# Kernel optimization log

Measured on AMD Instinct MI355X. Metric: run time of the kernel, lower is better.

The kernel has to match this reference:

```python
import jax, jax.numpy as jnp
import numpy as np

E, S, L, H, C = 32, 64, 20, 512, 32  # episodes, steps, max_comm_len, hidden_size, comm_shape
STD_MIN, STD_MAX = 2.0611536e-09, 7.389056  # exp(-20), exp(2)


def setup_inputs() -> dict:
    key = jax.random.key(0)
    ks = jax.random.split(key, 12)
    def p(k, shape):
        return jax.random.normal(k, shape, jnp.float32) * 0.02
    return {
        'x': jax.random.normal(ks[0], (E, S, H), jnp.float32),
        'Wr': p(ks[1], (2 * H, H)), 'br': jnp.zeros((H,), jnp.float32),
        'Wz': p(ks[2], (2 * H, H)), 'bz': jnp.zeros((H,), jnp.float32),
        'Wn': p(ks[3], (2 * H, H)), 'bn': jnp.zeros((H,), jnp.float32),
        'conv_w1': p(ks[4], (H // 4, H, 1)), 'conv_b1': jnp.zeros((H // 4,), jnp.float32),
        'conv_w3': p(ks[5], (H // 4, H, 3)), 'conv_b3': jnp.zeros((H // 4,), jnp.float32),
        'conv_w5': p(ks[6], (H // 4, H, 5)), 'conv_b5': jnp.zeros((H // 4,), jnp.float32),
        'conv_w7': p(ks[7], (H // 4, H, 7)), 'conv_b7': jnp.zeros((H // 4,), jnp.float32),
        'prelu_a': jnp.asarray(0.25, jnp.float32),
        'W_mu': p(ks[8], (H, C)), 'b_mu': jnp.zeros((C,), jnp.float32),
        'W_std': p(ks[9], (H, C)), 'b_std': jnp.zeros((C,), jnp.float32),
        'eps': jax.random.normal(ks[10], (E, S, L, C), jnp.float32),
    }


def reference(x, Wr, br, Wz, bz, Wn, bn,
              conv_w1, conv_b1, conv_w3, conv_b3, conv_w5, conv_b5, conv_w7, conv_b7,
              prelu_a, W_mu, b_mu, W_std, b_std, eps):
    B = E * S
    xf = x.reshape(B, H)  # same input fed to the RNN at every comm step

    def step(h, _):
        xh = jnp.concatenate([xf, h], -1)
        r = jax.nn.sigmoid(xh @ Wr + br)
        z = jax.nn.sigmoid(xh @ Wz + bz)
        n = jnp.tanh(jnp.concatenate([xf, r * h], -1) @ Wn + bn)
        h_new = (1.0 - z) * n + z * h  # time_constant=1 -> h = new GRU state
        return h_new, h_new

    h0 = jnp.zeros((B, H), x.dtype)
    _, hs = jax.lax.scan(step, h0, None, length=L)  # (L, B, H)
    comm_h = jnp.transpose(hs, (1, 2, 0))  # (B, H, L) -- NCW layout for conv

    dn = ('NCH', 'OIH', 'NCH')
    def conv(w, b, k):
        pad = (k - 1) // 2
        y = jax.lax.conv_general_dilated(comm_h, w, (1,), [(pad, pad)], dimension_numbers=dn)
        return y + b[None, :, None]

    y = jnp.concatenate([
        conv(conv_w1, conv_b1, 1),
        conv(conv_w3, conv_b3, 3),
        conv(conv_w5, conv_b5, 5),
        conv(conv_w7, conv_b7, 7),
    ], axis=1)  # (B, H, L)
    y = jnp.where(y >= 0, y, prelu_a * y)  # PReLU; dropout is identity in eval
    y = jnp.transpose(y, (0, 2, 1)).reshape(E, S, L, H)

    mu = y @ W_mu + b_mu
    std = jnp.clip(jax.nn.softplus(y @ W_std + b_std), STD_MIN, STD_MAX)
    comm = mu + eps * std  # reparameterized Normal sample
    comm_out = jnp.tanh(comm)
    log2pi = jnp.asarray(np.log(2.0 * np.pi), jnp.float32)
    log_prob = (-0.5 * ((comm - mu) / std) ** 2 - jnp.log(std) - 0.5 * log2pi
                - jnp.log(1.0 - comm_out ** 2 + 1e-6))
    log_prob = jnp.mean(log_prob, -1, keepdims=True)  # (E,S,L,1)
    log_prob = jnp.mean(log_prob, -2)  # (E,S,1)
    return comm_out, log_prob
```

## Files before the change

kernel.cpp:

```cpp
#include <hip/hip_runtime.h>
#include <hip/hip_bf16.h>

typedef __hip_bfloat16 bf16;
typedef short short8 __attribute__((ext_vector_type(8)));
typedef float floatx4 __attribute__((ext_vector_type(4)));

#define BDIM 2048
#define HDIM 512
#define LDIM 20
#define CDIM 32
#define LSTR 40

__device__ __forceinline__ float sigm(float x) { return 1.0f / (1.0f + expf(-x)); }

__device__ __forceinline__ void ll16(const short* g, short* l)
{
    __builtin_amdgcn_global_load_lds(
        (const __attribute__((address_space(1))) void*)g,
        (__attribute__((address_space(3))) void*)l, 16, 0, 0);
}
#define WAITVM(N) asm volatile("s_waitcnt vmcnt(" #N ")" ::: "memory")

__device__ __forceinline__ void gemm_tile_k(
    const short* __restrict__ A, int lda,
    const short* __restrict__ Bt, int ldb,
    int K, short* lds, floatx4 (&acc)[4][4], int tid)
{
    short* As = lds;
    short* Bs = lds + 128 * LSTR;
    const int wave = tid >> 6, lane = tid & 63;
    const int wm = wave & 1, wn = wave >> 1;
    const int m16 = lane & 15, quad = lane >> 4;
    const int r0 = tid >> 2;
    const int koff = (tid & 3) * 8;

    short8 a0 = *(const short8*)(A + (size_t)r0 * lda + koff);
    short8 a1 = *(const short8*)(A + (size_t)(r0 + 64) * lda + koff);
    short8 b0 = *(const short8*)(Bt + (size_t)r0 * ldb + koff);
    short8 b1 = *(const short8*)(Bt + (size_t)(r0 + 64) * ldb + koff);
    for (int k0 = 0; k0 < K; k0 += 32) {
        __syncthreads();
        *(short8*)(As + r0 * LSTR + koff) = a0;
        *(short8*)(As + (r0 + 64) * LSTR + koff) = a1;
        *(short8*)(Bs + r0 * LSTR + koff) = b0;
        *(short8*)(Bs + (r0 + 64) * LSTR + koff) = b1;
        __syncthreads();
        if (k0 + 32 < K) {
            a0 = *(const short8*)(A + (size_t)r0 * lda + k0 + 32 + koff);
            a1 = *(const short8*)(A + (size_t)(r0 + 64) * lda + k0 + 32 + koff);
            b0 = *(const short8*)(Bt + (size_t)r0 * ldb + k0 + 32 + koff);
            b1 = *(const short8*)(Bt + (size_t)(r0 + 64) * ldb + k0 + 32 + koff);
        }
        short8 af[4], bfr[4];
#pragma unroll
        for (int i = 0; i < 4; ++i)
            af[i] = *(short8*)(As + (wm * 64 + i * 16 + m16) * LSTR + quad * 8);
#pragma unroll
        for (int j = 0; j < 4; ++j)
            bfr[j] = *(short8*)(Bs + (wn * 64 + j * 16 + m16) * LSTR + quad * 8);
#pragma unroll
        for (int i = 0; i < 4; ++i)
#pragma unroll
            for (int j = 0; j < 4; ++j)
                acc[i][j] = __builtin_amdgcn_mfma_f32_16x16x32_bf16(
                    af[i], bfr[j], acc[i][j], 0, 0, 0);
    }
}

__device__ __forceinline__ void gemm_tile_k256(
    const short* __restrict__ A,
    const short* __restrict__ Bt,
    short* lds, floatx4 (&acc)[4][4], int tid)
{
    short* As = lds;
    short* Bs = lds + 256 * LSTR;
    const int wave = tid >> 6, lane = tid & 63;
    const int wm = wave & 3, wn = wave >> 2;
    const int m16 = lane & 15, quad = lane >> 4;
    const int r0 = tid >> 2;
    const int koff = (tid & 3) * 8;

    short8 a0 = *(const short8*)(A + (size_t)r0 * 512 + koff);
    short8 a1 = *(const short8*)(A + (size_t)(r0 + 128) * 512 + koff);
    short8 b0 = *(const short8*)(Bt + (size_t)r0 * 512 + koff);
    for (int k0 = 0; k0 < 512; k0 += 32) {
        __syncthreads();
        *(short8*)(As + r0 * LSTR + koff) = a0;
        *(short8*)(As + (r0 + 128) * LSTR + koff) = a1;
        *(short8*)(Bs + r0 * LSTR + koff) = b0;
        __syncthreads();
        if (k0 + 32 < 512) {
            a0 = *(const short8*)(A + (size_t)r0 * 512 + k0 + 32 + koff);
            a1 = *(const short8*)(A + (size_t)(r0 + 128) * 512 + k0 + 32 + koff);
            b0 = *(const short8*)(Bt + (size_t)r0 * 512 + k0 + 32 + koff);
        }
        short8 af[4], bfr[4];
#pragma unroll
        for (int i = 0; i < 4; ++i)
            af[i] = *(short8*)(As + (wm * 64 + i * 16 + m16) * LSTR + quad * 8);
#pragma unroll
        for (int j = 0; j < 4; ++j)
            bfr[j] = *(short8*)(Bs + (wn * 64 + j * 16 + m16) * LSTR + quad * 8);
#pragma unroll
        for (int i = 0; i < 4; ++i)
#pragma unroll
            for (int j = 0; j < 4; ++j)
                acc[i][j] = __builtin_amdgcn_mfma_f32_16x16x32_bf16(
                    af[i], bfr[j], acc[i][j], 0, 0, 0);
    }
}

__global__ __launch_bounds__(256) void k_prep_xb(const float* __restrict__ x,
                                                 bf16* __restrict__ xb)
{
    int i = blockIdx.x * 256 + threadIdx.x;
    xb[i] = (bf16)x[i];
}

__global__ __launch_bounds__(256) void k_transpose_512(const float* __restrict__ src,
                                                       bf16* __restrict__ dst)
{
    __shared__ float tile[32][33];
    int tx = threadIdx.x & 31, ty = threadIdx.x >> 5;
    int k0 = blockIdx.x * 32, n0 = blockIdx.y * 32;
#pragma unroll
    for (int i = 0; i < 32; i += 8)
        tile[ty + i][tx] = src[(size_t)(k0 + ty + i) * 512 + n0 + tx];
    __syncthreads();
#pragma unroll
    for (int i = 0; i < 32; i += 8)
        dst[(size_t)(n0 + ty + i) * 512 + k0 + tx] = (bf16)tile[tx][ty + i];
}

__global__ __launch_bounds__(256) void k_swzW(const float* __restrict__ Wr,
                                              const float* __restrict__ Wz,
                                              const float* __restrict__ Wn,
                                              bf16* __restrict__ Wfrag)
{
    int idx = blockIdx.x * 256 + threadIdx.x;
    int e = idx & 7, lane = (idx >> 3) & 63;
    int t2 = idx >> 9;
    int f = t2 % 6, jk = t2 / 6;
    int kc = jk & 15, j = jk >> 4;
    int ftype = f >> 1;
    int col = j * 32 + (f & 1) * 16 + (lane & 15);
    int k = kc * 32 + ((lane >> 4) << 3) + e;
    const float* W = (ftype == 0) ? Wr : (ftype == 1) ? Wz : Wn;
    Wfrag[idx] = (bf16)W[(size_t)(512 + k) * 512 + col];
}

__global__ __launch_bounds__(256) void k_prep_wc(
    const float* __restrict__ w1, const float* __restrict__ w3,
    const float* __restrict__ w5, const float* __restrict__ w7,
    bf16* __restrict__ wt)
{
    int idx = blockIdx.x * 256 + threadIdx.x;
    int g, base;
    if (idx < 65536)       { g = 0; base = 0;      }
    else if (idx < 262144) { g = 1; base = 65536;  }
    else if (idx < 589824) { g = 2; base = 262144; }
    else                   { g = 3; base = 589824; }
    int rel = idx - base;
    int k = 2 * g + 1;
    int ci = rel & 511;
    int t2 = rel >> 9;
    int co = t2 & 127;
    int tap = t2 >> 7;
    const float* w = (g == 0) ? w1 : (g == 1) ? w3 : (g == 2) ? w5 : w7;
    wt[idx] = (bf16)w[((size_t)co * 512 + ci) * k + tap];
}

__global__ __launch_bounds__(256) void k_prep_wh(const float* __restrict__ Wmu,
                                                 const float* __restrict__ Wstd,
                                                 bf16* __restrict__ Wh_t)
{
    int idx = blockIdx.x * 256 + threadIdx.x;
    int n = idx >> 9, k = idx & 511;
    float v = (n < 32) ? Wmu[(size_t)k * 32 + n] : Wstd[(size_t)k * 32 + (n - 32)];
    Wh_t[idx] = (bf16)v;
}

__global__ __launch_bounds__(256) void k_gx(
    const bf16* __restrict__ xb, const bf16* __restrict__ Wx_t,
    const float* __restrict__ br, const float* __restrict__ bz,
    const float* __restrict__ bn, bf16* __restrict__ gxb)
{
    __shared__ short lds[2 * 128 * LSTR];
    const int tid = threadIdx.x;
    const int row0 = blockIdx.x * 128, col0 = blockIdx.y * 128;
    floatx4 acc[4][4];
#pragma unroll
    for (int i = 0; i < 4; ++i)
#pragma unroll
        for (int j = 0; j < 4; ++j) acc[i][j] = (floatx4)0.0f;
    gemm_tile_k((const short*)xb + (size_t)row0 * 512, 512,
                (const short*)Wx_t + (size_t)col0 * 512, 512, 512, lds, acc, tid);
    const int wave = tid >> 6, lane = tid & 63;
    const int wm = wave & 1, wn = wave >> 1;
    const int m16 = lane & 15, quad = lane >> 4;
#pragma unroll
    for (int i = 0; i < 4; ++i)
#pragma unroll
        for (int j = 0; j < 4; ++j)
#pragma unroll
            for (int reg = 0; reg < 4; ++reg) {
                int b = row0 + wm * 64 + i * 16 + quad * 4 + reg;
                int n = col0 + wn * 64 + j * 16 + m16;
                float bias = (n < 512) ? br[n] : (n < 1024) ? bz[n - 512] : bn[n - 1024];
                gxb[(size_t)b * 1536 + n] = (bf16)(acc[i][j][reg] + bias);
            }
}

__device__ __forceinline__ void gbar2(unsigned* flags, int j, unsigned target,
                                      bool fast, int tid)
{
    WAITVM(0);
    __syncthreads();
    if (tid < 64) {
        if (tid == 0) {
            if (!fast) __threadfence();
            __hip_atomic_store(flags + j, target, __ATOMIC_RELAXED,
                               __HIP_MEMORY_SCOPE_AGENT);
        }
        unsigned v; int guard = 0;
        do {
            v = (tid < 16) ? __hip_atomic_load(flags + tid, __ATOMIC_RELAXED,
                                               __HIP_MEMORY_SCOPE_AGENT)
                           : target;
        } while (__ballot(v >= target) != ~0ull && ++guard < (1 << 20));
        if (!fast) { if (tid == 0) __threadfence(); }
        else asm volatile("buffer_inv" ::: "memory");
    }
    __syncthreads();
}

template<int NF>
__device__ __forceinline__ void phase_reg(
    const short* __restrict__ srcw, const short* __restrict__ wl,
    int f0, int lane, floatx4 (&acc)[NF])
{
    const short* g = srcw + (size_t)(lane & 15) * 512 + (lane >> 4) * 8;
    short8 a[16];
#pragma unroll
    for (int kc = 0; kc < 16; ++kc)
        a[kc] = *(const short8*)(g + kc * 32);
#pragma unroll
    for (int kc = 0; kc < 16; ++kc) {
        short8 bfr[NF];
#pragma unroll
        for (int f = 0; f < NF; ++f)
            bfr[f] = *(short8*)(wl + ((kc * 6 + f0 + f) << 9) + lane * 8);
#pragma unroll
        for (int f = 0; f < NF; ++f)
            acc[f] = __builtin_amdgcn_mfma_f32_16x16x32_bf16(a[kc], bfr[f],
                                                             acc[f], 0, 0, 0);
    }
}

__global__ __launch_bounds__(512, 2) void k_gru9(
    const bf16* __restrict__ Wfrag, const bf16* __restrict__ gxb,
    bf16* __restrict__ hs, bf16* __restrict__ rhb,
    unsigned* __restrict__ ctr, int* __restrict__ xcdtab)
{
    __shared__ short wlds[6 * 16 * 512];
    const int tid = threadIdx.x;
    const int wave = tid >> 6, lane = tid & 63;
    const int m16 = lane & 15, quad = lane >> 4;
    const int b = blockIdx.x;
    const int s = b >> 3;
    const int m = (b & 7) + ((s & 1) << 3);
    const int j = s >> 1;
    const int wrow = wave * 16;
    unsigned* flg  = ctr + m * 32;
    unsigned* vflg = ctr + m * 32 + 16;

    int myxcd;
    asm volatile("s_getreg_b32 %0, hwreg(HW_REG_XCC_ID)" : "=s"(myxcd));
    myxcd &= 15;
    if (tid == 0) xcdtab[m * 16 + j] = myxcd;

    const short* wsrc = (const short*)Wfrag + (size_t)j * 49152;
#pragma unroll
    for (int r = 0; r < 12; ++r)
        ll16(wsrc + ((wave * 12 + r) << 9) + lane * 8, wlds + ((wave * 12 + r) << 9));

    float gxr[2][4], gxz[2][4], gxn[2][4];
#pragma unroll
    for (int reg = 0; reg < 4; ++reg) {
        const bf16* gp = gxb + (size_t)(m * 128 + wrow + quad * 4 + reg) * 1536 + j * 32;
#pragma unroll
        for (int fc = 0; fc < 2; ++fc) {
            int c = fc * 16 + m16;
            gxr[fc][reg] = __bfloat162float(gp[c]);
            gxz[fc][reg] = __bfloat162float(gp[512 + c]);
            gxn[fc][reg] = __bfloat162float(gp[1024 + c]);
        }
    }

    gbar2(vflg, j, 1u, false, tid);
    bool fast = true;
#pragma unroll
    for (int jj = 0; jj < 16; ++jj) {
        int xv = __hip_atomic_load((const int*)xcdtab + m * 16 + jj,
                                   __ATOMIC_RELAXED, __HIP_MEMORY_SCOPE_AGENT);
        fast = fast && (xv == myxcd);
    }

    float h32[2][4];
    float zf[2][4];
    unsigned nbar = 0;
    const int rowg = m * 128 + wrow + quad * 4;

#pragma unroll
    for (int fc = 0; fc < 2; ++fc)
#pragma unroll
        for (int reg = 0; reg < 4; ++reg) {
            float z = sigm(gxz[fc][reg]);
            float nv = tanhf(gxn[fc][reg]);
            float hn = (1.0f - z) * nv;
            h32[fc][reg] = hn;
            hs[(size_t)(rowg + reg) * 512 + j * 32 + fc * 16 + m16] = (bf16)hn;
        }
    ++nbar; gbar2(flg, j, nbar, fast, tid);

    for (int t = 1; t < LDIM; ++t) {
        floatx4 acc[4];
#pragma unroll
        for (int f = 0; f < 4; ++f) acc[f] = (floatx4)0.0f;
        phase_reg<4>((const short*)hs + ((size_t)(t - 1) * BDIM + m * 128 + wrow) * 512,
                     wlds, 0, lane, acc);
#pragma unroll
        for (int fc = 0; fc < 2; ++fc)
#pragma unroll
            for (int reg = 0; reg < 4; ++reg) {
                float r = sigm(acc[fc][reg] + gxr[fc][reg]);
                zf[fc][reg] = sigm(acc[2 + fc][reg] + gxz[fc][reg]);
                rhb[(size_t)(rowg + reg) * 512 + j * 32 + fc * 16 + m16] =
                    (bf16)(r * h32[fc][reg]);
            }
        ++nbar; gbar2(flg, j, nbar, fast, tid);
        floatx4 acc2[2];
#pragma unroll
        for (int f = 0; f < 2; ++f) acc2[f] = (floatx4)0.0f;
        phase_reg<2>((const short*)rhb + (size_t)(m * 128 + wrow) * 512,
                     wlds, 4, lane, acc2);
#pragma unroll
        for (int fc = 0; fc < 2; ++fc)
#pragma unroll
            for (int reg = 0; reg < 4; ++reg) {
                float nv = tanhf(acc2[fc][reg] + gxn[fc][reg]);
                float z = zf[fc][reg];
                float hn = (1.0f - z) * nv + z * h32[fc][reg];
                h32[fc][reg] = hn;
                hs[((size_t)t * BDIM + rowg + reg) * 512 + j * 32 + fc * 16 + m16] =
                    (bf16)hn;
            }
        if (t < LDIM - 1) { ++nbar; gbar2(flg, j, nbar, fast, tid); }
    }
}

__global__ __launch_bounds__(512, 2) void k_conv(
    const bf16* __restrict__ hs, const bf16* __restrict__ Wc_t,
    const float* __restrict__ b1, const float* __restrict__ b3,
    const float* __restrict__ b5, const float* __restrict__ b7,
    const float* __restrict__ pa, bf16* __restrict__ y)
{
    __shared__ short lds[(256 + 128) * LSTR];
    const int tid = threadIdx.x;
    const int btile = blockIdx.x, g = blockIdx.y, l = blockIdx.z;
    const int row0 = btile * 256;
    const int ktap = 2 * g + 1, p = g;
    const int offs[4] = {0, 65536, 262144, 589824};
    const short* Wg = (const short*)Wc_t + offs[g];
    floatx4 acc[4][4];
#pragma unroll
    for (int i = 0; i < 4; ++i)
#pragma unroll
        for (int j = 0; j < 4; ++j) acc[i][j] = (floatx4)0.0f;
    for (int tap = 0; tap < ktap; ++tap) {
        int li = l + tap - p;
        if (li < 0 || li >= LDIM) continue;
        gemm_tile_k256((const short*)hs + (size_t)li * BDIM * HDIM + (size_t)row0 * 512,
                       Wg + (size_t)tap * 128 * 512, lds, acc, tid);
    }
    const float* bp = (g == 0) ? b1 : (g == 1) ? b3 : (g == 2) ? b5 : b7;
    const float a = *pa;
    const int wave = tid >> 6, lane = tid & 63;
    const int wm = wave & 3, wn = wave >> 2;
    const int m16 = lane & 15, quad = lane >> 4;
#pragma unroll
    for (int i = 0; i < 4; ++i)
#pragma unroll
        for (int j = 0; j < 4; ++j)
#pragma unroll
            for (int reg = 0; reg < 4; ++reg) {
                int b = row0 + wm * 64 + i * 16 + quad * 4 + reg;
                int col = wn * 64 + j * 16 + m16;
                float v = acc[i][j][reg] + bp[col];
                v = (v >= 0.0f) ? v : a * v;
                y[((size_t)b * LDIM + l) * 512 + g * 128 + col] = (bf16)v;
            }
}

__global__ __launch_bounds__(256) void k_head2(
    const bf16* __restrict__ y, const bf16* __restrict__ Wh_t,
    const float* __restrict__ bmu, const float* __restrict__ bstd,
    const float* __restrict__ eps, float* __restrict__ out_comm,
    float* __restrict__ lpsum)
{
    __shared__ short As[128 * LSTR];
    __shared__ short Bs[64 * LSTR];
    const int tid = threadIdx.x;
    const int wave = tid >> 6, lane = tid & 63;
    const int m16 = lane & 15, quad = lane >> 4;
    const int r0 = tid >> 2, koff = (tid & 3) * 8;
    const int row0 = blockIdx.x * 128;
    floatx4 acc[2][4];
#pragma unroll
    for (int i = 0; i < 2; ++i)
#pragma unroll
        for (int j = 0; j < 4; ++j) acc[i][j] = (floatx4)0.0f;
    const short* Ap = (const short*)y + (size_t)row0 * 512;
    const short* Bp = (const short*)Wh_t;
    short8 ga0 = *(const short8*)(Ap + (size_t)r0 * 512 + koff);
    short8 ga1 = *(const short8*)(Ap + (size_t)(r0 + 64) * 512 + koff);
    short8 gb0 = *(const short8*)(Bp + (size_t)r0 * 512 + koff);
    for (int k0 = 0; k0 < 512; k0 += 32) {
        __syncthreads();
        *(short8*)(As + r0 * LSTR + koff) = ga0;
        *(short8*)(As + (r0 + 64) * LSTR + koff) = ga1;
        *(short8*)(Bs + r0 * LSTR + koff) = gb0;
        __syncthreads();
        if (k0 + 32 < 512) {
            ga0 = *(const short8*)(Ap + (size_t)r0 * 512 + k0 + 32 + koff);
            ga1 = *(const short8*)(Ap + (size_t)(r0 + 64) * 512 + k0 + 32 + koff);
            gb0 = *(const short8*)(Bp + (size_t)r0 * 512 + k0 + 32 + koff);
        }
        short8 af[2], bfr[4];
#pragma unroll
        for (int i = 0; i < 2; ++i)
            af[i] = *(short8*)(As + (wave * 32 + i * 16 + m16) * LSTR + quad * 8);
#pragma unroll
        for (int j = 0; j < 4; ++j)
            bfr[j] = *(short8*)(Bs + (j * 16 + m16) * LSTR + quad * 8);
#pragma unroll
        for (int i = 0; i < 2; ++i)
#pragma unroll
            for (int j = 0; j < 4; ++j)
                acc[i][j] = __builtin_amdgcn_mfma_f32_16x16x32_bf16(
                    af[i], bfr[j], acc[i][j], 0, 0, 0);
    }
#pragma unroll
    for (int i = 0; i < 2; ++i)
#pragma unroll
        for (int reg = 0; reg < 4; ++reg) {
            int row = row0 + wave * 32 + i * 16 + quad * 4 + reg;
            float lp = 0.0f;
#pragma unroll
            for (int jj = 0; jj < 2; ++jj) {
                int c = jj * 16 + m16;
                float mu = acc[i][jj][reg] + bmu[c];
                float sraw = acc[i][jj + 2][reg] + bstd[c];
                float sp = (sraw > 20.0f) ? sraw : log1pf(expf(sraw));
                float sd = fminf(fmaxf(sp, 2.0611536e-09f), 7.389056f);
                float e = eps[(size_t)row * 32 + c];
                float comm = fmaf(e, sd, mu);
                float tt = tanhf(comm);
                out_comm[(size_t)row * 32 + c] = tt;
                lp += -0.5f * e * e - logf(sd) - 0.91893853320467274f
                      - logf(1.0f - tt * tt + 1e-6f);
            }
            lp += __shfl_xor(lp, 1, 16);
            lp += __shfl_xor(lp, 2, 16);
            lp += __shfl_xor(lp, 4, 16);
            lp += __shfl_xor(lp, 8, 16);
            if (m16 == 0) lpsum[row] = lp;
        }
}

__global__ __launch_bounds__(256) void k_final(const float* __restrict__ lpsum,
                                               float* __restrict__ out2)
{
    int b = blockIdx.x * 256 + threadIdx.x;
    if (b < BDIM) {
        float s = 0.0f;
#pragma unroll
        for (int i = 0; i < LDIM; ++i) s += lpsum[b * LDIM + i];
        out2[b] = s * (1.0f / (LDIM * CDIM));
    }
}

extern "C" void kernel_launch(void* const* d_in, const int* in_sizes, int n_in,
                              void* d_out, int out_size, void* d_ws, size_t ws_size,
                              hipStream_t stream)
{
    const float* x    = (const float*)d_in[0];
    const float* Wr   = (const float*)d_in[1];
    const float* br   = (const float*)d_in[2];
    const float* Wz   = (const float*)d_in[3];
    const float* bz   = (const float*)d_in[4];
    const float* Wn   = (const float*)d_in[5];
    const float* bn   = (const float*)d_in[6];
    const float* w1   = (const float*)d_in[7];
    const float* b1   = (const float*)d_in[8];
    const float* w3   = (const float*)d_in[9];
    const float* b3   = (const float*)d_in[10];
    const float* w5   = (const float*)d_in[11];
    const float* b5   = (const float*)d_in[12];
    const float* w7   = (const float*)d_in[13];
    const float* b7   = (const float*)d_in[14];
    const float* pa   = (const float*)d_in[15];
    const float* Wmu  = (const float*)d_in[16];
    const float* bmu  = (const float*)d_in[17];
    const float* Wstd = (const float*)d_in[18];
    const float* bstd = (const float*)d_in[19];
    const float* eps  = (const float*)d_in[20];

    char* cur = (char*)d_ws;
    auto alloc = [&](size_t bytes) -> void* {
        void* r = (void*)cur;
        cur += (bytes + 255) & ~(size_t)255;
        return r;
    };
    const size_t BH = (size_t)BDIM * HDIM;
    bf16*  gxb   = (bf16*)alloc((size_t)BDIM * 1536 * 2);
    bf16*  xb    = (bf16*)alloc(BH * 2);
    bf16*  hs    = (bf16*)alloc(BH * LDIM * 2);
    bf16*  ybuf  = (bf16*)alloc(BH * LDIM * 2);
    bf16*  Wx_t  = (bf16*)alloc((size_t)1536 * 512 * 2);
    bf16*  Wfrag = (bf16*)alloc((size_t)786432 * 2);
    bf16*  Wc_t  = (bf16*)alloc((size_t)1048576 * 2);
    bf16*  Wh_t  = (bf16*)alloc((size_t)64 * 512 * 2);
    bf16*  rhb   = (bf16*)alloc((size_t)BDIM * 512 * 2);
    float* lpsum = (float*)alloc((size_t)BDIM * LDIM * 4);
    unsigned* ctr = (unsigned*)alloc(2048);
    int*   xcdtab = (int*)alloc(1024);

    hipMemsetAsync(ctr, 0, 2048, stream);

    k_prep_xb<<<4096, 256, 0, stream>>>(x, xb);
    dim3 tg(16, 16);
    k_transpose_512<<<tg, 256, 0, stream>>>(Wr, Wx_t);
    k_transpose_512<<<tg, 256, 0, stream>>>(Wz, Wx_t + 262144);
    k_transpose_512<<<tg, 256, 0, stream>>>(Wn, Wx_t + 524288);
    k_swzW<<<3072, 256, 0, stream>>>(Wr, Wz, Wn, Wfrag);
    k_prep_wc<<<4096, 256, 0, stream>>>(w1, w3, w5, w7, Wc_t);
    k_prep_wh<<<128, 256, 0, stream>>>(Wmu, Wstd, Wh_t);

    k_gx<<<dim3(16, 12), 256, 0, stream>>>(xb, Wx_t, br, bz, bn, gxb);

    k_gru9<<<256, 512, 0, stream>>>(Wfrag, gxb, hs, rhb, ctr, xcdtab);

    k_conv<<<dim3(8, 4, 20), 512, 0, stream>>>(hs, Wc_t, b1, b3, b5, b7, pa, ybuf);

    float* out_comm = (float*)d_out;
    float* out_lp   = (float*)d_out + (size_t)BDIM * LDIM * CDIM;
    k_head2<<<320, 256, 0, stream>>>(ybuf, Wh_t, bmu, bstd, eps, out_comm, lpsum);
    k_final<<<8, 256, 0, stream>>>(lpsum, out_lp);
}
```

Baseline: 537.9 us.

## Merge prep kernels, use direct global-to-LDS loads, retile conv to 128-row blocks

Six weight and input prep launches are folded into one multi-role kernel plus one 3D transpose launch, which cuts launch overhead. The GEMM tile helper now copies global memory straight into unpadded LDS with global_load_lds instead of staging through registers. It waits for the loads before each compute step, so the previous register prefetch overlap is gone. The conv kernel switches from 256-row/512-thread blocks to 128-row/256-thread blocks with twice the grid, and the barrier spin-guard limit is lowered.

```diff
diff --git a/kernel.cpp b/kernel.cpp
--- a/kernel.cpp
+++ b/kernel.cpp
@@ -21,43 +21,36 @@
 }
 #define WAITVM(N) asm volatile("s_waitcnt vmcnt(" #N ")" ::: "memory")
 
-__device__ __forceinline__ void gemm_tile_k(
+__device__ __forceinline__ void gemm_tile_ll(
     const short* __restrict__ A, int lda,
     const short* __restrict__ Bt, int ldb,
     int K, short* lds, floatx4 (&acc)[4][4], int tid)
 {
     short* As = lds;
-    short* Bs = lds + 128 * LSTR;
+    short* Bs = lds + 128 * 32;
     const int wave = tid >> 6, lane = tid & 63;
     const int wm = wave & 1, wn = wave >> 1;
     const int m16 = lane & 15, quad = lane >> 4;
-    const int r0 = tid >> 2;
-    const int koff = (tid & 3) * 8;
-
-    short8 a0 = *(const short8*)(A + (size_t)r0 * lda + koff);
-    short8 a1 = *(const short8*)(A + (size_t)(r0 + 64) * lda + koff);
-    short8 b0 = *(const short8*)(Bt + (size_t)r0 * ldb + koff);
-    short8 b1 = *(const short8*)(Bt + (size_t)(r0 + 64) * ldb + koff);
+    const int lrow = lane >> 2;
+    const int lcol = (lane & 3) * 8;
+
     for (int k0 = 0; k0 < K; k0 += 32) {
         __syncthreads();
-        *(short8*)(As + r0 * LSTR + koff) = a0;
-        *(short8*)(As + (r0 + 64) * LSTR + koff) = a1;
-        *(short8*)(Bs + r0 * LSTR + koff) = b0;
-        *(short8*)(Bs + (r0 + 64) * LSTR + koff) = b1;
+#pragma unroll
+        for (int seg = 0; seg < 2; ++seg) {
+            const int sg = wave + seg * 4;
+            ll16(A  + (size_t)(sg * 16 + lrow) * lda + k0 + lcol, As + sg * 512);
+            ll16(Bt + (size_t)(sg * 16 + lrow) * ldb + k0 + lcol, Bs + sg * 512);
+        }
+        WAITVM(0);
         __syncthreads();
-        if (k0 + 32 < K) {
-            a0 = *(const short8*)(A + (size_t)r0 * lda + k0 + 32 + koff);
-            a1 = *(const short8*)(A + (size_t)(r0 + 64) * lda + k0 + 32 + koff);
-            b0 = *(const short8*)(Bt + (size_t)r0 * ldb + k0 + 32 + koff);
-            b1 = *(const short8*)(Bt + (size_t)(r0 + 64) * ldb + k0 + 32 + koff);
-        }
         short8 af[4], bfr[4];
 #pragma unroll
         for (int i = 0; i < 4; ++i)
-            af[i] = *(short8*)(As + (wm * 64 + i * 16 + m16) * LSTR + quad * 8);
+            af[i] = *(short8*)(As + (wm * 64 + i * 16 + m16) * 32 + quad * 8);
 #pragma unroll
         for (int j = 0; j < 4; ++j)
-            bfr[j] = *(short8*)(Bs + (wn * 64 + j * 16 + m16) * LSTR + quad * 8);
+            bfr[j] = *(short8*)(Bs + (wn * 64 + j * 16 + m16) * 32 + quad * 8);
 #pragma unroll
         for (int i = 0; i < 4; ++i)
 #pragma unroll
@@ -67,60 +60,62 @@
     }
 }
 
-__device__ __forceinline__ void gemm_tile_k256(
-    const short* __restrict__ A,
-    const short* __restrict__ Bt,
-    short* lds, floatx4 (&acc)[4][4], int tid)
-{
-    short* As = lds;
-    short* Bs = lds + 256 * LSTR;
-    const int wave = tid >> 6, lane = tid & 63;
-    const int wm = wave & 3, wn = wave >> 2;
-    const int m16 = lane & 15, quad = lane >> 4;
-    const int r0 = tid >> 2;
-    const int koff = (tid & 3) * 8;
-
-    short8 a0 = *(const short8*)(A + (size_t)r0 * 512 + koff);
-    short8 a1 = *(const short8*)(A + (size_t)(r0 + 128) * 512 + koff);
-    short8 b0 = *(const short8*)(Bt + (size_t)r0 * 512 + koff);
-    for (int k0 = 0; k0 < 512; k0 += 32) {
-        __syncthreads();
-        *(short8*)(As + r0 * LSTR + koff) = a0;
-        *(short8*)(As + (r0 + 128) * LSTR + koff) = a1;
-        *(short8*)(Bs + r0 * LSTR + koff) = b0;
-        __syncthreads();
-        if (k0 + 32 < 512) {
-            a0 = *(const short8*)(A + (size_t)r0 * 512 + k0 + 32 + koff);
-            a1 = *(const short8*)(A + (size_t)(r0 + 128) * 512 + k0 + 32 + koff);
-            b0 = *(const short8*)(Bt + (size_t)r0 * 512 + k0 + 32 + koff);
-        }
-        short8 af[4], bfr[4];
-#pragma unroll
-        for (int i = 0; i < 4; ++i)
-            af[i] = *(short8*)(As + (wm * 64 + i * 16 + m16) * LSTR + quad * 8);
-#pragma unroll
-        for (int j = 0; j < 4; ++j)
-            bfr[j] = *(short8*)(Bs + (wn * 64 + j * 16 + m16) * LSTR + quad * 8);
-#pragma unroll
-        for (int i = 0; i < 4; ++i)
-#pragma unroll
-            for (int j = 0; j < 4; ++j)
-                acc[i][j] = __builtin_amdgcn_mfma_f32_16x16x32_bf16(
-                    af[i], bfr[j], acc[i][j], 0, 0, 0);
-    }
-}
-
-__global__ __launch_bounds__(256) void k_prep_xb(const float* __restrict__ x,
-                                                 bf16* __restrict__ xb)
-{
-    int i = blockIdx.x * 256 + threadIdx.x;
-    xb[i] = (bf16)x[i];
-}
-
-__global__ __launch_bounds__(256) void k_transpose_512(const float* __restrict__ src,
-                                                       bf16* __restrict__ dst)
+__global__ __launch_bounds__(256) void k_prep_all(
+    const float* __restrict__ x, bf16* __restrict__ xb,
+    const float* __restrict__ Wr, const float* __restrict__ Wz,
+    const float* __restrict__ Wn, bf16* __restrict__ Wfrag,
+    const float* __restrict__ w1, const float* __restrict__ w3,
+    const float* __restrict__ w5, const float* __restrict__ w7,
+    bf16* __restrict__ wt,
+    const float* __restrict__ Wmu, const float* __restrict__ Wstd,
+    bf16* __restrict__ Wh_t)
+{
+    const int bid = blockIdx.x, tid = threadIdx.x;
+    if (bid < 4096) {
+        int i = bid * 256 + tid;
+        xb[i] = (bf16)x[i];
+    } else if (bid < 7168) {
+        int idx = (bid - 4096) * 256 + tid;
+        int e = idx & 7, lane = (idx >> 3) & 63;
+        int t2 = idx >> 9;
+        int f = t2 % 6, jk = t2 / 6;
+        int kc = jk & 15, j = jk >> 4;
+        int ftype = f >> 1;
+        int col = j * 32 + (f & 1) * 16 + (lane & 15);
+        int k = kc * 32 + ((lane >> 4) << 3) + e;
+        const float* W = (ftype == 0) ? Wr : (ftype == 1) ? Wz : Wn;
+        Wfrag[idx] = (bf16)W[(size_t)(512 + k) * 512 + col];
+    } else if (bid < 11264) {
+        int idx = (bid - 7168) * 256 + tid;
+        int g, base;
+        if (idx < 65536)       { g = 0; base = 0;      }
+        else if (idx < 262144) { g = 1; base = 65536;  }
+        else if (idx < 589824) { g = 2; base = 262144; }
+        else                   { g = 3; base = 589824; }
+        int rel = idx - base;
+        int k = 2 * g + 1;
+        int ci = rel & 511;
+        int t2 = rel >> 9;
+        int co = t2 & 127;
+        int tap = t2 >> 7;
+        const float* w = (g == 0) ? w1 : (g == 1) ? w3 : (g == 2) ? w5 : w7;
+        wt[idx] = (bf16)w[((size_t)co * 512 + ci) * k + tap];
+    } else {
+        int idx = (bid - 11264) * 256 + tid;
+        int n = idx >> 9, k = idx & 511;
+        float v = (n < 32) ? Wmu[(size_t)k * 32 + n]
+                           : Wstd[(size_t)k * 32 + (n - 32)];
+        Wh_t[idx] = (bf16)v;
+    }
+}
+
+__global__ __launch_bounds__(256) void k_transpose3(
+    const float* __restrict__ Wr, const float* __restrict__ Wz,
+    const float* __restrict__ Wn, bf16* __restrict__ dst)
 {
     __shared__ float tile[32][33];
+    const float* src = (blockIdx.z == 0) ? Wr : (blockIdx.z == 1) ? Wz : Wn;
+    bf16* d = dst + (size_t)blockIdx.z * 262144;
     int tx = threadIdx.x & 31, ty = threadIdx.x >> 5;
     int k0 = blockIdx.x * 32, n0 = blockIdx.y * 32;
 #pragma unroll
@@ -129,55 +124,7 @@
     __syncthreads();
 #pragma unroll
     for (int i = 0; i < 32; i += 8)
-        dst[(size_t)(n0 + ty + i) * 512 + k0 + tx] = (bf16)tile[tx][ty + i];
-}
-
-__global__ __launch_bounds__(256) void k_swzW(const float* __restrict__ Wr,
-                                              const float* __restrict__ Wz,
-                                              const float* __restrict__ Wn,
-                                              bf16* __restrict__ Wfrag)
-{
-    int idx = blockIdx.x * 256 + threadIdx.x;
-    int e = idx & 7, lane = (idx >> 3) & 63;
-    int t2 = idx >> 9;
-    int f = t2 % 6, jk = t2 / 6;
-    int kc = jk & 15, j = jk >> 4;
-    int ftype = f >> 1;
-    int col = j * 32 + (f & 1) * 16 + (lane & 15);
-    int k = kc * 32 + ((lane >> 4) << 3) + e;
-    const float* W = (ftype == 0) ? Wr : (ftype == 1) ? Wz : Wn;
-    Wfrag[idx] = (bf16)W[(size_t)(512 + k) * 512 + col];
-}
-
-__global__ __launch_bounds__(256) void k_prep_wc(
-    const float* __restrict__ w1, const float* __restrict__ w3,
-    const float* __restrict__ w5, const float* __restrict__ w7,
-    bf16* __restrict__ wt)
-{
-    int idx = blockIdx.x * 256 + threadIdx.x;
-    int g, base;
-    if (idx < 65536)       { g = 0; base = 0;      }
-    else if (idx < 262144) { g = 1; base = 65536;  }
-    else if (idx < 589824) { g = 2; base = 262144; }
-    else                   { g = 3; base = 589824; }
-    int rel = idx - base;
-    int k = 2 * g + 1;
-    int ci = rel & 511;
-    int t2 = rel >> 9;
-    int co = t2 & 127;
-    int tap = t2 >> 7;
-    const float* w = (g == 0) ? w1 : (g == 1) ? w3 : (g == 2) ? w5 : w7;
-    wt[idx] = (bf16)w[((size_t)co * 512 + ci) * k + tap];
-}
-
-__global__ __launch_bounds__(256) void k_prep_wh(const float* __restrict__ Wmu,
-                                                 const float* __restrict__ Wstd,
-                                                 bf16* __restrict__ Wh_t)
-{
-    int idx = blockIdx.x * 256 + threadIdx.x;
-    int n = idx >> 9, k = idx & 511;
-    float v = (n < 32) ? Wmu[(size_t)k * 32 + n] : Wstd[(size_t)k * 32 + (n - 32)];
-    Wh_t[idx] = (bf16)v;
+        d[(size_t)(n0 + ty + i) * 512 + k0 + tx] = (bf16)tile[tx][ty + i];
 }
 
 __global__ __launch_bounds__(256) void k_gx(
@@ -185,7 +132,7 @@
     const float* __restrict__ br, const float* __restrict__ bz,
     const float* __restrict__ bn, bf16* __restrict__ gxb)
 {
-    __shared__ short lds[2 * 128 * LSTR];
+    __shared__ short lds[2 * 128 * 32];
     const int tid = threadIdx.x;
     const int row0 = blockIdx.x * 128, col0 = blockIdx.y * 128;
     floatx4 acc[4][4];
@@ -193,8 +140,8 @@
     for (int i = 0; i < 4; ++i)
 #pragma unroll
         for (int j = 0; j < 4; ++j) acc[i][j] = (floatx4)0.0f;
-    gemm_tile_k((const short*)xb + (size_t)row0 * 512, 512,
-                (const short*)Wx_t + (size_t)col0 * 512, 512, 512, lds, acc, tid);
+    gemm_tile_ll((const short*)xb + (size_t)row0 * 512, 512,
+                 (const short*)Wx_t + (size_t)col0 * 512, 512, 512, lds, acc, tid);
     const int wave = tid >> 6, lane = tid & 63;
     const int wm = wave & 1, wn = wave >> 1;
     const int m16 = lane & 15, quad = lane >> 4;
@@ -227,7 +174,7 @@
             v = (tid < 16) ? __hip_atomic_load(flags + tid, __ATOMIC_RELAXED,
                                                __HIP_MEMORY_SCOPE_AGENT)
                            : target;
-        } while (__ballot(v >= target) != ~0ull && ++guard < (1 << 20));
+        } while (__ballot(v >= target) != ~0ull && ++guard < (1 << 18));
         if (!fast) { if (tid == 0) __threadfence(); }
         else asm volatile("buffer_inv" ::: "memory");
     }
@@ -359,16 +306,16 @@
     }
 }
 
-__global__ __launch_bounds__(512, 2) void k_conv(
+__global__ __launch_bounds__(256) void k_conv(
     const bf16* __restrict__ hs, const bf16* __restrict__ Wc_t,
     const float* __restrict__ b1, const float* __restrict__ b3,
     const float* __restrict__ b5, const float* __restrict__ b7,
     const float* __restrict__ pa, bf16* __restrict__ y)
 {
-    __shared__ short lds[(256 + 128) * LSTR];
+    __shared__ short lds[2 * 128 * 32];
     const int tid = threadIdx.x;
     const int btile = blockIdx.x, g = blockIdx.y, l = blockIdx.z;
-    const int row0 = btile * 256;
+    const int row0 = btile * 128;
     const int ktap = 2 * g + 1, p = g;
     const int offs[4] = {0, 65536, 262144, 589824};
     const short* Wg = (const short*)Wc_t + offs[g];
@@ -380,13 +327,13 @@
     for (int tap = 0; tap < ktap; ++tap) {
         int li = l + tap - p;
         if (li < 0 || li >= LDIM) continue;
-        gemm_tile_k256((const short*)hs + (size_t)li * BDIM * HDIM + (size_t)row0 * 512,
-                       Wg + (size_t)tap * 128 * 512, lds, acc, tid);
+        gemm_tile_ll((const short*)hs + (size_t)li * BDIM * HDIM + (size_t)row0 * 512, 512,
+                     Wg + (size_t)tap * 128 * 512, 512, 512, lds, acc, tid);
     }
     const float* bp = (g == 0) ? b1 : (g == 1) ? b3 : (g == 2) ? b5 : b7;
     const float a = *pa;
     const int wave = tid >> 6, lane = tid & 63;
-    const int wm = wave & 3, wn = wave >> 2;
+    const int wm = wave & 1, wn = wave >> 1;
     const int m16 = lane & 15, quad = lane >> 4;
 #pragma unroll
     for (int i = 0; i < 4; ++i)
@@ -538,20 +485,15 @@
 
     hipMemsetAsync(ctr, 0, 2048, stream);
 
-    k_prep_xb<<<4096, 256, 0, stream>>>(x, xb);
-    dim3 tg(16, 16);
-    k_transpose_512<<<tg, 256, 0, stream>>>(Wr, Wx_t);
-    k_transpose_512<<<tg, 256, 0, stream>>>(Wz, Wx_t + 262144);
-    k_transpose_512<<<tg, 256, 0, stream>>>(Wn, Wx_t + 524288);
-    k_swzW<<<3072, 256, 0, stream>>>(Wr, Wz, Wn, Wfrag);
-    k_prep_wc<<<4096, 256, 0, stream>>>(w1, w3, w5, w7, Wc_t);
-    k_prep_wh<<<128, 256, 0, stream>>>(Wmu, Wstd, Wh_t);
+    k_prep_all<<<11392, 256, 0, stream>>>(x, xb, Wr, Wz, Wn, Wfrag,
+                                          w1, w3, w5, w7, Wc_t, Wmu, Wstd, Wh_t);
+    k_transpose3<<<dim3(16, 16, 3), 256, 0, stream>>>(Wr, Wz, Wn, Wx_t);
 
     k_gx<<<dim3(16, 12), 256, 0, stream>>>(xb, Wx_t, br, bz, bn, gxb);
 
     k_gru9<<<256, 512, 0, stream>>>(Wfrag, gxb, hs, rhb, ctr, xcdtab);
 
-    k_conv<<<dim3(8, 4, 20), 512, 0, stream>>>(hs, Wc_t, b1, b3, b5, b7, pa, ybuf);
+    k_conv<<<dim3(16, 4, 20), 256, 0, stream>>>(hs, Wc_t, b1, b3, b5, b7, pa, ybuf);
 
     float* out_comm = (float*)d_out;
     float* out_lp   = (float*)d_out + (size_t)BDIM * LDIM * CDIM;
```

Result: faster. 506.6 us (-5.8%).
